# Optimization experiments

Measured on AMD Instinct MI355X. Metric: run time of the kernel, lower is better.

## Reference

```python
import jax, jax.numpy as jnp
import numpy as np
from jax.scipy.special import logsumexp

TAU = 0.07
LAMBDA_LL = 1.0
LAMBDA_GL = 0.5
LAMBDA_SMOOTH = 0.1
NEG_INF = -jnp.inf


def setup_inputs() -> dict:
    key = jax.random.key(0)
    k1, k2, k3, k4 = jax.random.split(key, 4)
    B, L, D, K = 16, 32, 256, 131072
    return {
        "z_t": jax.random.normal(k1, (B, L, D), dtype=jnp.float32),
        "g": jax.random.normal(k2, (B, D), dtype=jnp.float32),
        "va_values": jax.random.uniform(k3, (B, L, 2), dtype=jnp.float32),
        "memory_queue": jax.random.normal(k4, (K, D), dtype=jnp.float32),
    }


def _combined_loss(z_t, g, memory_queue):
    B, L, D = z_t.shape
    N = B * L
    z = z_t.reshape(N, D)

    # ---- Global-Local loss: anchor g[b], positive z_t[b,t], negatives = frames of other clips + queue
    sim_gz = (g @ z.T) / TAU                      # [B, N]
    pos_gl = sim_gz.reshape(B, B, L)[jnp.arange(B), jnp.arange(B)]  # [B, L]
    col_batch = jnp.arange(N) // L                # batch id of each frame column
    neg_gl = jnp.where(col_batch[None, :] == jnp.arange(B)[:, None], NEG_INF, sim_gz)  # [B, N]
    q_gl = (g @ memory_queue.T) / TAU             # [B, K]
    lse_neg_gl = jnp.logaddexp(logsumexp(neg_gl, axis=1), logsumexp(q_gl, axis=1))     # [B]
    loss_gl = jnp.mean(jnp.logaddexp(pos_gl, lse_neg_gl[:, None]) - pos_gl)

    # ---- Local-Local loss: anchor (b,t), positive (b,t+1), negatives = all other frames + queue
    anchor_idx = (jnp.arange(B)[:, None] * L + jnp.arange(L - 1)[None, :]).reshape(-1)  # [M]
    M = anchor_idx.shape[0]
    sim_zz = (z @ z.T) / TAU                      # [N, N]
    rows = sim_zz[anchor_idx]                     # [M, N]
    pos_ll = sim_zz[anchor_idx, anchor_idx + 1]   # [M]
    r = jnp.arange(M)
    neg_rows = rows.at[r, anchor_idx].set(NEG_INF).at[r, anchor_idx + 1].set(NEG_INF)
    q_ll = (z[anchor_idx] @ memory_queue.T) / TAU  # [M, K] -- dominant memory traffic
    lse_neg_ll = jnp.logaddexp(logsumexp(neg_rows, axis=1), logsumexp(q_ll, axis=1))
    loss_ll = jnp.mean(jnp.logaddexp(pos_ll, lse_neg_ll) - pos_ll)
    # NOTE: the VA-derived positive weight in the original code is applied after
    # the logits are built, so it has no effect on the loss; reproduced faithfully.

    # ---- Smoothness loss
    diff = z_t[:, 1:, :] - z_t[:, :-1, :]
    loss_smooth = jnp.mean(jnp.sum(diff * diff, axis=-1))

    total = LAMBDA_LL * loss_ll + LAMBDA_GL * loss_gl + LAMBDA_SMOOTH * loss_smooth
    return total


def reference(z_t, g, va_values, memory_queue):
    # va_values is unused by the effective math (see note in _combined_loss)
    return _combined_loss(z_t, g, memory_queue)
```

## Files before the change

kernel.cpp:

```cpp
#include <hip/hip_runtime.h>
#include <hip/hip_bf16.h>

#define D_ 256
#define NROWS_Z 512
#define NROWS 528
#define KQ 131072
#define NBLK 256
#define NBLK_BIG 512
#define KC 512
#define SUBT 32
#define SCALE_A (14.285714285714286f * 1.4426950408889634f)
#define LN2 0.6931471805599453f

typedef __attribute__((ext_vector_type(8))) short short8;
typedef __attribute__((ext_vector_type(4))) float f32x4;

__device__ __forceinline__ float exp2fast(float x) {
  float r; asm("v_exp_f32 %0, %1" : "=v"(r) : "v"(x)); return r;
}
__device__ __forceinline__ float log2fast(float x) {
  float r; asm("v_log_f32 %0, %1" : "=v"(r) : "v"(x)); return r;
}

__device__ __forceinline__ short bf16r(float x) {
  union { float f; unsigned u; } c; c.f = x;
  unsigned r = (c.u + 0x7fffu + ((c.u >> 16) & 1u)) >> 16;
  return (short)r;
}

__device__ __forceinline__ void merge_ms(float& m, float& s, float m2, float s2) {
  float mm = fmaxf(m, m2);
  s = s * exp2fast(m - mm) + s2 * exp2fast(m2 - mm);
  m = mm;
}

__device__ __forceinline__ void upd(float& m, float& s, float v) {
  float d = v - m;
  if (__builtin_expect(__any(d > 8.f), 0)) {
    const float mn = fmaxf(m, v);
    s *= exp2fast(m - mn);
    m = mn; d = v - m;
  }
  s += exp2fast(d);
}

__device__ __forceinline__ short8 cvt8(float4 a, float4 b) {
  union { unsigned u[4]; short8 s; } o;
  asm("v_cvt_pk_bf16_f32 %0, %1, %2" : "=v"(o.u[0]) : "v"(a.x), "v"(a.y));
  asm("v_cvt_pk_bf16_f32 %0, %1, %2" : "=v"(o.u[1]) : "v"(a.z), "v"(a.w));
  asm("v_cvt_pk_bf16_f32 %0, %1, %2" : "=v"(o.u[2]) : "v"(b.x), "v"(b.y));
  asm("v_cvt_pk_bf16_f32 %0, %1, %2" : "=v"(o.u[3]) : "v"(b.z), "v"(b.w));
  return o.s;
}

__global__ void prep_kernel(const float* __restrict__ z, const float* __restrict__ g,
                            short* __restrict__ Abf, short* __restrict__ Zp,
                            float* __restrict__ smoothp) {
  const int r = blockIdx.x, d = threadIdx.x;
  const float v = (r < NROWS_Z) ? z[r * D_ + d] : g[(r - NROWS_Z) * D_ + d];
  Abf[r * D_ + d] = bf16r(v * SCALE_A);
  if (r < NROWS_Z) {
    Zp[r * D_ + d] = bf16r(v);
    float acc = 0.f;
    if ((r & 31) != 31) { const float dv = z[(r + 1) * D_ + d] - v; acc = dv * dv; }
#pragma unroll
    for (int mask = 1; mask < 64; mask <<= 1) acc += __shfl_xor(acc, mask);
    __shared__ float red[4];
    if ((d & 63) == 0) red[d >> 6] = acc;
    __syncthreads();
    if (d == 0) smoothp[r] = red[0] + red[1] + red[2] + red[3];
  }
}

__global__ __launch_bounds__(512, 2) void big_kernel(
    const float* __restrict__ queue, const short* __restrict__ Abf,
    float2* __restrict__ zpart, float2* __restrict__ gpart) {
  const int tid = threadIdx.x;
  const int chunk = blockIdx.x & 255;
  const int rowgroup = blockIdx.x >> 8;
  const int wid = tid >> 6, lane = tid & 63;
  const int l15 = lane & 15, l4 = lane >> 4;

  __shared__ __align__(16) char qs[2][16 * 512];
  __shared__ float2 gbuf[8 * 16];

  short8 afrag[2][8];
#pragma unroll
  for (int s = 0; s < 2; ++s) {
    const short* base = Abf + (rowgroup * 256 + wid * 32 + s * 16 + l15) * D_ + l4 * 8;
#pragma unroll
    for (int k = 0; k < 8; ++k) afrag[s][k] = *(const short8*)(base + k * 32);
  }
  const short* gbase = Abf + (NROWS_Z + l15) * D_ + l4 * 8;

  float mz[2][4], sz[2][4];
#pragma unroll
  for (int s = 0; s < 2; ++s)
#pragma unroll
    for (int r = 0; r < 4; ++r) { mz[s][r] = -1e30f; sz[s][r] = 0.f; }
  float mg[4], sg[4];
#pragma unroll
  for (int r = 0; r < 4; ++r) { mg[r] = -1e30f; sg[r] = 0.f; }

  const int srow = tid >> 5;
  const int sslot = tid & 31;
  const int woff = srow * 512 + (((sslot ^ srow) & 31) << 4);
  const float* qbase = queue + (size_t)(chunk * KC + srow) * D_ + sslot * 8;

  const f32x4 fz = {0.f, 0.f, 0.f, 0.f};
  const bool dog = (rowgroup == 0);

  float4 fa0 = *(const float4*)qbase;
  float4 fa1 = *(const float4*)(qbase + 4);
  float4 fb0 = *(const float4*)(qbase + 16 * D_);
  float4 fb1 = *(const float4*)(qbase + 16 * D_ + 4);
  *(short8*)(qs[0] + woff) = cvt8(fa0, fa1);
  __syncthreads();

#define COMPUTE(BUF, ST)                                                              \
  {                                                                                   \
    const char* qb = qs[BUF];                                                         \
    f32x4 acc0 = fz, acc1 = fz;                                                       \
    if (dog && ((ST) & 7) == wid) {                                                   \
      f32x4 accg = fz;                                                                \
      _Pragma("unroll")                                                               \
      for (int k = 0; k < 8; ++k) {                                                   \
        const short8 bf = *(const short8*)(qb + l15 * 512 + ((((k * 4 + l4) ^ l15) & 31) << 4)); \
        acc0 = __builtin_amdgcn_mfma_f32_16x16x32_bf16(afrag[0][k], bf, acc0, 0, 0, 0); \
        acc1 = __builtin_amdgcn_mfma_f32_16x16x32_bf16(afrag[1][k], bf, acc1, 0, 0, 0); \
        const short8 ag = *(const short8*)(gbase + k * 32);                           \
        accg = __builtin_amdgcn_mfma_f32_16x16x32_bf16(ag, bf, accg, 0, 0, 0);        \
      }                                                                               \
      _Pragma("unroll")                                                               \
      for (int r = 0; r < 4; ++r) upd(mg[r], sg[r], accg[r]);                         \
    } else {                                                                          \
      _Pragma("unroll")                                                               \
      for (int k = 0; k < 8; ++k) {                                                   \
        const short8 bf = *(const short8*)(qb + l15 * 512 + ((((k * 4 + l4) ^ l15) & 31) << 4)); \
        acc0 = __builtin_amdgcn_mfma_f32_16x16x32_bf16(afrag[0][k], bf, acc0, 0, 0, 0); \
        acc1 = __builtin_amdgcn_mfma_f32_16x16x32_bf16(afrag[1][k], bf, acc1, 0, 0, 0); \
      }                                                                               \
    }                                                                                 \
    _Pragma("unroll")                                                                 \
    for (int r = 0; r < 4; ++r) upd(mz[0][r], sz[0][r], acc0[r]);                     \
    _Pragma("unroll")                                                                 \
    for (int r = 0; r < 4; ++r) upd(mz[1][r], sz[1][r], acc1[r]);                     \
  }

  for (int st = 0; st < SUBT; st += 2) {
    if (st + 2 < SUBT) {
      const float* qp = qbase + (st + 2) * (16 * D_);
      fa0 = *(const float4*)qp;
      fa1 = *(const float4*)(qp + 4);
    }
    *(short8*)(qs[1] + woff) = cvt8(fb0, fb1);
    COMPUTE(0, st)
    __syncthreads();

    if (st + 3 < SUBT) {
      const float* qp = qbase + (st + 3) * (16 * D_);
      fb0 = *(const float4*)qp;
      fb1 = *(const float4*)(qp + 4);
    }
    if (st + 2 < SUBT) *(short8*)(qs[0] + woff) = cvt8(fa0, fa1);
    COMPUTE(1, st + 1)
    __syncthreads();
  }

#pragma unroll
  for (int s = 0; s < 2; ++s)
#pragma unroll
    for (int r = 0; r < 4; ++r) {
#pragma unroll
      for (int mask = 1; mask < 16; mask <<= 1) {
        const float om = __shfl_xor(mz[s][r], mask);
        const float os = __shfl_xor(sz[s][r], mask);
        merge_ms(mz[s][r], sz[s][r], om, os);
      }
    }

  if (l15 == 0) {
#pragma unroll
    for (int s = 0; s < 2; ++s)
#pragma unroll
      for (int r = 0; r < 4; ++r) {
        const int row = rowgroup * 256 + wid * 32 + s * 16 + l4 * 4 + r;
        zpart[row * NBLK + chunk] = make_float2(mz[s][r], sz[s][r]);
      }
  }

  if (dog) {
#pragma unroll
    for (int r = 0; r < 4; ++r) {
#pragma unroll
      for (int mask = 1; mask < 16; mask <<= 1) {
        const float om = __shfl_xor(mg[r], mask);
        const float os = __shfl_xor(sg[r], mask);
        merge_ms(mg[r], sg[r], om, os);
      }
    }
    if (l15 == 0) {
#pragma unroll
      for (int r = 0; r < 4; ++r)
        gbuf[wid * 16 + l4 * 4 + r] = make_float2(mg[r], sg[r]);
    }
    __syncthreads();
    if (tid < 16) {
      float m = gbuf[tid].x, s = gbuf[tid].y;
      for (int w = 1; w < 8; ++w) merge_ms(m, s, gbuf[w * 16 + tid].x, gbuf[w * 16 + tid].y);
      gpart[tid * NBLK + chunk] = make_float2(m, s);
    }
  }
}

__global__ __launch_bounds__(512) void zmm_kernel(
    const short* __restrict__ Abf, const short* __restrict__ Zp,
    float2* __restrict__ zcol, float* __restrict__ posll, float* __restrict__ posgl) {
  const int tid = threadIdx.x;
  const int wid = tid >> 6, lane = tid & 63;
  const int l15 = lane & 15, l4 = lane >> 4;
  const int r0 = blockIdx.x * 16;

  short8 af[8];
#pragma unroll
  for (int k = 0; k < 8; ++k)
    af[k] = *(const short8*)(Abf + (r0 + l15) * D_ + l4 * 8 + k * 32);

  float m[4], s[4];
#pragma unroll
  for (int r = 0; r < 4; ++r) { m[r] = -1e30f; s[r] = 0.f; }

  for (int st = 0; st < 4; ++st) {
    const int c0 = wid * 64 + st * 16;
    const f32x4 fz = {0.f, 0.f, 0.f, 0.f};
    f32x4 acc = fz;
#pragma unroll
    for (int k = 0; k < 8; ++k) {
      const short8 bq = *(const short8*)(Zp + (c0 + l15) * D_ + l4 * 8 + k * 32);
      acc = __builtin_amdgcn_mfma_f32_16x16x32_bf16(af[k], bq, acc, 0, 0, 0);
    }
#pragma unroll
    for (int r = 0; r < 4; ++r) {
      const int row = r0 + l4 * 4 + r;
      const int col = c0 + l15;
      const float v = acc[r];
      bool masked;
      if (r0 < NROWS_Z) {
        if (col == row + 1) posll[row] = v * LN2;
        masked = (col == row) || (col == row + 1);
      } else {
        const int b = row - NROWS_Z;
        const bool own = ((col >> 5) == b);
        if (own) posgl[col] = v * LN2;
        masked = own;
      }
      if (!masked) upd(m[r], s[r], v);
    }
  }
#pragma unroll
  for (int r = 0; r < 4; ++r) {
#pragma unroll
    for (int mask = 1; mask < 16; mask <<= 1) {
      const float om = __shfl_xor(m[r], mask);
      const float os = __shfl_xor(s[r], mask);
      merge_ms(m[r], s[r], om, os);
    }
  }
  __shared__ float2 lds[8][16];
  if (l15 == 0) {
#pragma unroll
    for (int r = 0; r < 4; ++r) lds[wid][l4 * 4 + r] = make_float2(m[r], s[r]);
  }
  __syncthreads();
  if (tid < 16) {
    float mm = lds[0][tid].x, ss = lds[0][tid].y;
    for (int w = 1; w < 8; ++w) merge_ms(mm, ss, lds[w][tid].x, lds[w][tid].y);
    zcol[r0 + tid] = make_float2(mm, ss);
  }
}

__global__ void reduce_kernel(const float2* __restrict__ zpart, const float2* __restrict__ gpart,
                              const float2* __restrict__ zcol, float* __restrict__ lse_row) {
  const int r = blockIdx.x, tid = threadIdx.x;
  const float2 p = (r < NROWS_Z) ? zpart[r * NBLK + tid] : gpart[(r - NROWS_Z) * NBLK + tid];
  float m = p.x, s = p.y;
  __shared__ float2 red[4];
#pragma unroll
  for (int mask = 1; mask < 64; mask <<= 1) {
    const float om = __shfl_xor(m, mask);
    const float os = __shfl_xor(s, mask);
    merge_ms(m, s, om, os);
  }
  if ((tid & 63) == 0) red[tid >> 6] = make_float2(m, s);
  __syncthreads();
  if (tid == 0) {
    for (int w = 1; w < 4; ++w) merge_ms(m, s, red[w].x, red[w].y);
    const float2 zc = zcol[r];
    merge_ms(m, s, zc.x, zc.y);
    lse_row[r] = LN2 * (m + log2fast(s));
  }
}

__global__ void final_kernel(const float* __restrict__ lse_row, const float* __restrict__ posll,
                             const float* __restrict__ posgl, const float* __restrict__ smoothp,
                             float* __restrict__ out) {
  const int tid = threadIdx.x;
  float a_ll = 0.f, a_gl = 0.f, a_sm = 0.f;
  for (int i = tid; i < 496; i += 256) {
    const int b = i / 31, t = i - b * 31;
    const int a = b * 32 + t;
    const float pos = posll[a], lse = lse_row[a];
    const float d = lse - pos;
    a_ll += (d > 0.f) ? d + log1pf(__expf(-d)) : log1pf(__expf(d));
  }
  for (int i = tid; i < 512; i += 256) {
    const float pos = posgl[i], lse = lse_row[NROWS_Z + (i >> 5)];
    const float d = lse - pos;
    a_gl += (d > 0.f) ? d + log1pf(__expf(-d)) : log1pf(__expf(d));
  }
  for (int i = tid; i < 512; i += 256) a_sm += smoothp[i];

  __shared__ float red[4];
  float sums[3] = {a_ll, a_gl, a_sm};
  float tot[3];
  for (int j = 0; j < 3; ++j) {
    float v = sums[j];
#pragma unroll
    for (int mask = 1; mask < 64; mask <<= 1) v += __shfl_xor(v, mask);
    __syncthreads();
    if ((tid & 63) == 0) red[tid >> 6] = v;
    __syncthreads();
    tot[j] = red[0] + red[1] + red[2] + red[3];
  }
  if (tid == 0)
    out[0] = tot[0] / 496.f + 0.5f * (tot[1] / 512.f) + 0.1f * (tot[2] / 496.f);
}

extern "C" void kernel_launch(void* const* d_in, const int* in_sizes, int n_in,
                              void* d_out, int out_size, void* d_ws, size_t ws_size,
                              hipStream_t stream) {
  const float* z = (const float*)d_in[0];
  const float* g = (const float*)d_in[1];
  const float* queue = (const float*)d_in[3];
  float* out = (float*)d_out;
  char* ws = (char*)d_ws;

  constexpr size_t OFF_A = 0;
  constexpr size_t OFF_ZP = OFF_A + 270336;
  constexpr size_t OFF_ZPART = OFF_ZP + 262144;
  constexpr size_t OFF_GPART = OFF_ZPART + 1048576;
  constexpr size_t OFF_ZCOL = OFF_GPART + 32768;
  constexpr size_t OFF_POSLL = OFF_ZCOL + 4224;
  constexpr size_t OFF_POSGL = OFF_POSLL + 2048;
  constexpr size_t OFF_SM = OFF_POSGL + 2048;
  constexpr size_t OFF_LSE = OFF_SM + 2048;

  short* Abf = (short*)(ws + OFF_A);
  short* Zp = (short*)(ws + OFF_ZP);
  float2* zpart = (float2*)(ws + OFF_ZPART);
  float2* gpart = (float2*)(ws + OFF_GPART);
  float2* zcol = (float2*)(ws + OFF_ZCOL);
  float* posll = (float*)(ws + OFF_POSLL);
  float* posgl = (float*)(ws + OFF_POSGL);
  float* smoothp = (float*)(ws + OFF_SM);
  float* lse_row = (float*)(ws + OFF_LSE);

  prep_kernel<<<NROWS, 256, 0, stream>>>(z, g, Abf, Zp, smoothp);
  big_kernel<<<NBLK_BIG, 512, 0, stream>>>(queue, Abf, zpart, gpart);
  zmm_kernel<<<33, 512, 0, stream>>>(Abf, Zp, zcol, posll, posgl);
  reduce_kernel<<<NROWS, 256, 0, stream>>>(zpart, gpart, zcol, lse_row);
  final_kernel<<<1, 256, 0, stream>>>(lse_row, posll, posgl, smoothp, out);
}
```

Baseline: 122.6 us.

## Switch queue GEMM to FP8 MFMA with all rows per block

The queue-logit GEMM now converts the queue and the scaled activations to FP8 and uses the fp8 MFMA instruction. Each block now covers all 512 z rows, where before two row groups each re-read the same queue chunk, so the queue is read from global memory only once. The g rows are computed alongside in every block. The zmm path reuses the scaled bf16 buffer and rescales its output, and the chunk count adapts to the workspace size. FP8 rounding of logits scaled by 1/tau risks accuracy loss in the logsumexp.

```diff
diff --git a/kernel.cpp b/kernel.cpp
--- a/kernel.cpp
+++ b/kernel.cpp
@@ -5,11 +5,8 @@
 #define NROWS_Z 512
 #define NROWS 528
 #define KQ 131072
-#define NBLK 256
-#define NBLK_BIG 512
-#define KC 512
-#define SUBT 32
-#define SCALE_A (14.285714285714286f * 1.4426950408889634f)
+#define SCALE_A 20.6099291041f
+#define INV_SCALE_A (1.0f / SCALE_A)
 #define LN2 0.6931471805599453f
 
 typedef __attribute__((ext_vector_type(8))) short short8;
@@ -26,6 +23,12 @@
   union { float f; unsigned u; } c; c.f = x;
   unsigned r = (c.u + 0x7fffu + ((c.u >> 16) & 1u)) >> 16;
   return (short)r;
+}
+
+__device__ __forceinline__ unsigned cvt2fp8(float a, float b) {
+  unsigned r;
+  asm("v_cvt_pk_fp8_f32 %0, %1, %2" : "=v"(r) : "v"(a), "v"(b));
+  return r & 0xFFFFu;
 }
 
 __device__ __forceinline__ void merge_ms(float& m, float& s, float m2, float s2) {
@@ -44,131 +47,131 @@
   s += exp2fast(d);
 }
 
-__device__ __forceinline__ short8 cvt8(float4 a, float4 b) {
-  union { unsigned u[4]; short8 s; } o;
-  asm("v_cvt_pk_bf16_f32 %0, %1, %2" : "=v"(o.u[0]) : "v"(a.x), "v"(a.y));
-  asm("v_cvt_pk_bf16_f32 %0, %1, %2" : "=v"(o.u[1]) : "v"(a.z), "v"(a.w));
-  asm("v_cvt_pk_bf16_f32 %0, %1, %2" : "=v"(o.u[2]) : "v"(b.x), "v"(b.y));
-  asm("v_cvt_pk_bf16_f32 %0, %1, %2" : "=v"(o.u[3]) : "v"(b.z), "v"(b.w));
-  return o.s;
-}
-
 __global__ void prep_kernel(const float* __restrict__ z, const float* __restrict__ g,
-                            short* __restrict__ Abf, short* __restrict__ Zp,
+                            short* __restrict__ Abf, char* __restrict__ Abf8,
                             float* __restrict__ smoothp) {
   const int r = blockIdx.x, d = threadIdx.x;
+  __shared__ float vals[256];
+  __shared__ float red[4];
   const float v = (r < NROWS_Z) ? z[r * D_ + d] : g[(r - NROWS_Z) * D_ + d];
-  Abf[r * D_ + d] = bf16r(v * SCALE_A);
-  if (r < NROWS_Z) {
-    Zp[r * D_ + d] = bf16r(v);
-    float acc = 0.f;
-    if ((r & 31) != 31) { const float dv = z[(r + 1) * D_ + d] - v; acc = dv * dv; }
-#pragma unroll
-    for (int mask = 1; mask < 64; mask <<= 1) acc += __shfl_xor(acc, mask);
-    __shared__ float red[4];
-    if ((d & 63) == 0) red[d >> 6] = acc;
-    __syncthreads();
-    if (d == 0) smoothp[r] = red[0] + red[1] + red[2] + red[3];
-  }
+  const float vs = v * SCALE_A;
+  Abf[r * D_ + d] = bf16r(vs);
+  vals[d] = vs;
+  float acc = 0.f;
+  if (r < NROWS_Z && (r & 31) != 31) { const float dv = z[(r + 1) * D_ + d] - v; acc = dv * dv; }
+#pragma unroll
+  for (int mask = 1; mask < 64; mask <<= 1) acc += __shfl_xor(acc, mask);
+  if ((d & 63) == 0) red[d >> 6] = acc;
+  __syncthreads();
+  if (d < 64) {
+    const float4 q = *(const float4*)(vals + d * 4);
+    const unsigned w = cvt2fp8(q.x, q.y) | (cvt2fp8(q.z, q.w) << 16);
+    *(unsigned*)(Abf8 + r * D_ + d * 4) = w;
+  }
+  if (d == 0 && r < NROWS_Z) smoothp[r] = red[0] + red[1] + red[2] + red[3];
 }
 
 __global__ __launch_bounds__(512, 2) void big_kernel(
-    const float* __restrict__ queue, const short* __restrict__ Abf,
-    float2* __restrict__ zpart, float2* __restrict__ gpart) {
-  const int tid = threadIdx.x;
-  const int chunk = blockIdx.x & 255;
-  const int rowgroup = blockIdx.x >> 8;
+    const float* __restrict__ queue, const char* __restrict__ Abf8,
+    float2* __restrict__ zpart, float2* __restrict__ gpart,
+    int nchunk, int subt) {
+  const int tid = threadIdx.x, blk = blockIdx.x;
   const int wid = tid >> 6, lane = tid & 63;
   const int l15 = lane & 15, l4 = lane >> 4;
-
-  __shared__ __align__(16) char qs[2][16 * 512];
-  __shared__ float2 gbuf[8 * 16];
-
-  short8 afrag[2][8];
-#pragma unroll
-  for (int s = 0; s < 2; ++s) {
-    const short* base = Abf + (rowgroup * 256 + wid * 32 + s * 16 + l15) * D_ + l4 * 8;
-#pragma unroll
-    for (int k = 0; k < 8; ++k) afrag[s][k] = *(const short8*)(base + k * 32);
-  }
-  const short* gbase = Abf + (NROWS_Z + l15) * D_ + l4 * 8;
-
-  float mz[2][4], sz[2][4];
-#pragma unroll
-  for (int s = 0; s < 2; ++s)
+  const int qrows = KQ / nchunk;
+
+  __shared__ __align__(16) char qs[2][16 * 256];
+  __shared__ float2 gbuf[8][16];
+
+  long afrag[4][8];
+#pragma unroll
+  for (int s = 0; s < 4; ++s) {
+    const char* base = Abf8 + (wid * 64 + s * 16 + l15) * D_ + l4 * 8;
+#pragma unroll
+    for (int k = 0; k < 8; ++k) afrag[s][k] = *(const long*)(base + k * 32);
+  }
+  const char* gBbase = Abf8 + (NROWS_Z + l15) * D_ + l4 * 8;
+
+  float mz[4][4], sz[4][4];
+#pragma unroll
+  for (int s = 0; s < 4; ++s)
 #pragma unroll
     for (int r = 0; r < 4; ++r) { mz[s][r] = -1e30f; sz[s][r] = 0.f; }
-  float mg[4], sg[4];
-#pragma unroll
-  for (int r = 0; r < 4; ++r) { mg[r] = -1e30f; sg[r] = 0.f; }
+  float mg = -1e30f, sg = 0.f;
 
   const int srow = tid >> 5;
   const int sslot = tid & 31;
-  const int woff = srow * 512 + (((sslot ^ srow) & 31) << 4);
-  const float* qbase = queue + (size_t)(chunk * KC + srow) * D_ + sslot * 8;
+  const int woff = srow * D_ + ((sslot ^ srow) << 3);
+  const float* qbase = queue + (size_t)(blk * qrows + srow) * D_ + sslot * 8;
 
   const f32x4 fz = {0.f, 0.f, 0.f, 0.f};
-  const bool dog = (rowgroup == 0);
-
-  float4 fa0 = *(const float4*)qbase;
-  float4 fa1 = *(const float4*)(qbase + 4);
-  float4 fb0 = *(const float4*)(qbase + 16 * D_);
-  float4 fb1 = *(const float4*)(qbase + 16 * D_ + 4);
-  *(short8*)(qs[0] + woff) = cvt8(fa0, fa1);
-  __syncthreads();
+
+#define STAGE(BUF)                                                                    \
+  {                                                                                   \
+    const unsigned w0 = cvt2fp8(fa0.x, fa0.y) | (cvt2fp8(fa0.z, fa0.w) << 16);        \
+    const unsigned w1 = cvt2fp8(fa1.x, fa1.y) | (cvt2fp8(fa1.z, fa1.w) << 16);        \
+    *(uint2*)(qs[BUF] + woff) = make_uint2(w0, w1);                                   \
+  }
 
 #define COMPUTE(BUF, ST)                                                              \
   {                                                                                   \
     const char* qb = qs[BUF];                                                         \
-    f32x4 acc0 = fz, acc1 = fz;                                                       \
-    if (dog && ((ST) & 7) == wid) {                                                   \
+    f32x4 acc0 = fz, acc1 = fz, acc2 = fz, acc3 = fz;                                 \
+    _Pragma("unroll")                                                                 \
+    for (int kk = 0; kk < 8; ++kk) {                                                  \
+      const long bf = *(const long*)(qb + l15 * D_ + (((kk * 4 + l4) ^ l15) << 3));   \
+      acc0 = __builtin_amdgcn_mfma_f32_16x16x32_fp8_fp8(afrag[0][kk], bf, acc0, 0, 0, 0); \
+      acc1 = __builtin_amdgcn_mfma_f32_16x16x32_fp8_fp8(afrag[1][kk], bf, acc1, 0, 0, 0); \
+      acc2 = __builtin_amdgcn_mfma_f32_16x16x32_fp8_fp8(afrag[2][kk], bf, acc2, 0, 0, 0); \
+      acc3 = __builtin_amdgcn_mfma_f32_16x16x32_fp8_fp8(afrag[3][kk], bf, acc3, 0, 0, 0); \
+    }                                                                                 \
+    _Pragma("unroll")                                                                 \
+    for (int r = 0; r < 4; ++r) {                                                     \
+      upd(mz[0][r], sz[0][r], acc0[r]);                                               \
+      upd(mz[1][r], sz[1][r], acc1[r]);                                               \
+      upd(mz[2][r], sz[2][r], acc2[r]);                                               \
+      upd(mz[3][r], sz[3][r], acc3[r]);                                               \
+    }                                                                                 \
+    if ((((ST) & 7)) == wid) {                                                        \
       f32x4 accg = fz;                                                                \
       _Pragma("unroll")                                                               \
-      for (int k = 0; k < 8; ++k) {                                                   \
-        const short8 bf = *(const short8*)(qb + l15 * 512 + ((((k * 4 + l4) ^ l15) & 31) << 4)); \
-        acc0 = __builtin_amdgcn_mfma_f32_16x16x32_bf16(afrag[0][k], bf, acc0, 0, 0, 0); \
-        acc1 = __builtin_amdgcn_mfma_f32_16x16x32_bf16(afrag[1][k], bf, acc1, 0, 0, 0); \
-        const short8 ag = *(const short8*)(gbase + k * 32);                           \
-        accg = __builtin_amdgcn_mfma_f32_16x16x32_bf16(ag, bf, accg, 0, 0, 0);        \
+      for (int kk = 0; kk < 8; ++kk) {                                                \
+        const long bf = *(const long*)(qb + l15 * D_ + (((kk * 4 + l4) ^ l15) << 3)); \
+        const long gb = *(const long*)(gBbase + kk * 32);                             \
+        accg = __builtin_amdgcn_mfma_f32_16x16x32_fp8_fp8(bf, gb, accg, 0, 0, 0);     \
       }                                                                               \
       _Pragma("unroll")                                                               \
-      for (int r = 0; r < 4; ++r) upd(mg[r], sg[r], accg[r]);                         \
-    } else {                                                                          \
-      _Pragma("unroll")                                                               \
-      for (int k = 0; k < 8; ++k) {                                                   \
-        const short8 bf = *(const short8*)(qb + l15 * 512 + ((((k * 4 + l4) ^ l15) & 31) << 4)); \
-        acc0 = __builtin_amdgcn_mfma_f32_16x16x32_bf16(afrag[0][k], bf, acc0, 0, 0, 0); \
-        acc1 = __builtin_amdgcn_mfma_f32_16x16x32_bf16(afrag[1][k], bf, acc1, 0, 0, 0); \
-      }                                                                               \
+      for (int r = 0; r < 4; ++r) upd(mg, sg, accg[r]);                               \
     }                                                                                 \
-    _Pragma("unroll")                                                                 \
-    for (int r = 0; r < 4; ++r) upd(mz[0][r], sz[0][r], acc0[r]);                     \
-    _Pragma("unroll")                                                                 \
-    for (int r = 0; r < 4; ++r) upd(mz[1][r], sz[1][r], acc1[r]);                     \
-  }
-
-  for (int st = 0; st < SUBT; st += 2) {
-    if (st + 2 < SUBT) {
-      const float* qp = qbase + (st + 2) * (16 * D_);
+  }
+
+  float4 fa0 = *(const float4*)qbase;
+  float4 fa1 = *(const float4*)(qbase + 4);
+  STAGE(0)
+  __syncthreads();
+
+  for (int st = 0; st < subt; st += 2) {
+    {
+      const float* qp = qbase + (size_t)(st + 1) * (16 * D_);
       fa0 = *(const float4*)qp;
       fa1 = *(const float4*)(qp + 4);
     }
-    *(short8*)(qs[1] + woff) = cvt8(fb0, fb1);
     COMPUTE(0, st)
+    STAGE(1)
     __syncthreads();
 
-    if (st + 3 < SUBT) {
-      const float* qp = qbase + (st + 3) * (16 * D_);
-      fb0 = *(const float4*)qp;
-      fb1 = *(const float4*)(qp + 4);
-    }
-    if (st + 2 < SUBT) *(short8*)(qs[0] + woff) = cvt8(fa0, fa1);
+    if (st + 2 < subt) {
+      const float* qp = qbase + (size_t)(st + 2) * (16 * D_);
+      fa0 = *(const float4*)qp;
+      fa1 = *(const float4*)(qp + 4);
+    }
     COMPUTE(1, st + 1)
+    if (st + 2 < subt) STAGE(0)
     __syncthreads();
   }
 
 #pragma unroll
-  for (int s = 0; s < 2; ++s)
+  for (int s = 0; s < 4; ++s)
 #pragma unroll
     for (int r = 0; r < 4; ++r) {
 #pragma unroll
@@ -178,43 +181,33 @@
         merge_ms(mz[s][r], sz[s][r], om, os);
       }
     }
-
   if (l15 == 0) {
 #pragma unroll
-    for (int s = 0; s < 2; ++s)
+    for (int s = 0; s < 4; ++s)
 #pragma unroll
       for (int r = 0; r < 4; ++r) {
-        const int row = rowgroup * 256 + wid * 32 + s * 16 + l4 * 4 + r;
-        zpart[row * NBLK + chunk] = make_float2(mz[s][r], sz[s][r]);
+        const int row = wid * 64 + s * 16 + l4 * 4 + r;
+        zpart[row * nchunk + blk] = make_float2(mz[s][r], sz[s][r]);
       }
   }
 
-  if (dog) {
-#pragma unroll
-    for (int r = 0; r < 4; ++r) {
-#pragma unroll
-      for (int mask = 1; mask < 16; mask <<= 1) {
-        const float om = __shfl_xor(mg[r], mask);
-        const float os = __shfl_xor(sg[r], mask);
-        merge_ms(mg[r], sg[r], om, os);
-      }
-    }
-    if (l15 == 0) {
-#pragma unroll
-      for (int r = 0; r < 4; ++r)
-        gbuf[wid * 16 + l4 * 4 + r] = make_float2(mg[r], sg[r]);
-    }
-    __syncthreads();
-    if (tid < 16) {
-      float m = gbuf[tid].x, s = gbuf[tid].y;
-      for (int w = 1; w < 8; ++w) merge_ms(m, s, gbuf[w * 16 + tid].x, gbuf[w * 16 + tid].y);
-      gpart[tid * NBLK + chunk] = make_float2(m, s);
-    }
+#pragma unroll
+  for (int mask = 16; mask < 64; mask <<= 1) {
+    const float om = __shfl_xor(mg, mask);
+    const float os = __shfl_xor(sg, mask);
+    merge_ms(mg, sg, om, os);
+  }
+  if (lane < 16) gbuf[wid][l15] = make_float2(mg, sg);
+  __syncthreads();
+  if (tid < 16) {
+    float m = gbuf[0][tid].x, s = gbuf[0][tid].y;
+    for (int w = 1; w < 8; ++w) merge_ms(m, s, gbuf[w][tid].x, gbuf[w][tid].y);
+    gpart[tid * nchunk + blk] = make_float2(m, s);
   }
 }
 
 __global__ __launch_bounds__(512) void zmm_kernel(
-    const short* __restrict__ Abf, const short* __restrict__ Zp,
+    const short* __restrict__ Abf,
     float2* __restrict__ zcol, float* __restrict__ posll, float* __restrict__ posgl) {
   const int tid = threadIdx.x;
   const int wid = tid >> 6, lane = tid & 63;
@@ -236,14 +229,14 @@
     f32x4 acc = fz;
 #pragma unroll
     for (int k = 0; k < 8; ++k) {
-      const short8 bq = *(const short8*)(Zp + (c0 + l15) * D_ + l4 * 8 + k * 32);
+      const short8 bq = *(const short8*)(Abf + (c0 + l15) * D_ + l4 * 8 + k * 32);
       acc = __builtin_amdgcn_mfma_f32_16x16x32_bf16(af[k], bq, acc, 0, 0, 0);
     }
 #pragma unroll
     for (int r = 0; r < 4; ++r) {
       const int row = r0 + l4 * 4 + r;
       const int col = c0 + l15;
-      const float v = acc[r];
+      const float v = acc[r] * INV_SCALE_A;
       bool masked;
       if (r0 < NROWS_Z) {
         if (col == row + 1) posll[row] = v * LN2;
@@ -280,11 +273,12 @@
 }
 
 __global__ void reduce_kernel(const float2* __restrict__ zpart, const float2* __restrict__ gpart,
-                              const float2* __restrict__ zcol, float* __restrict__ lse_row) {
+                              const float2* __restrict__ zcol, float* __restrict__ lse_row,
+                              int nchunk) {
   const int r = blockIdx.x, tid = threadIdx.x;
-  const float2 p = (r < NROWS_Z) ? zpart[r * NBLK + tid] : gpart[(r - NROWS_Z) * NBLK + tid];
+  const float2 p = (r < NROWS_Z) ? zpart[r * nchunk + tid] : gpart[(r - NROWS_Z) * nchunk + tid];
   float m = p.x, s = p.y;
-  __shared__ float2 red[4];
+  __shared__ float2 red[8];
 #pragma unroll
   for (int mask = 1; mask < 64; mask <<= 1) {
     const float om = __shfl_xor(m, mask);
@@ -294,7 +288,8 @@
   if ((tid & 63) == 0) red[tid >> 6] = make_float2(m, s);
   __syncthreads();
   if (tid == 0) {
-    for (int w = 1; w < 4; ++w) merge_ms(m, s, red[w].x, red[w].y);
+    const int nw = blockDim.x >> 6;
+    for (int w = 1; w < nw; ++w) merge_ms(m, s, red[w].x, red[w].y);
     const float2 zc = zcol[r];
     merge_ms(m, s, zc.x, zc.y);
     lse_row[r] = LN2 * (m + log2fast(s));
@@ -345,29 +340,35 @@
   float* out = (float*)d_out;
   char* ws = (char*)d_ws;
 
-  constexpr size_t OFF_A = 0;
-  constexpr size_t OFF_ZP = OFF_A + 270336;
-  constexpr size_t OFF_ZPART = OFF_ZP + 262144;
-  constexpr size_t OFF_GPART = OFF_ZPART + 1048576;
-  constexpr size_t OFF_ZCOL = OFF_GPART + 32768;
-  constexpr size_t OFF_POSLL = OFF_ZCOL + 4224;
-  constexpr size_t OFF_POSGL = OFF_POSLL + 2048;
-  constexpr size_t OFF_SM = OFF_POSGL + 2048;
-  constexpr size_t OFF_LSE = OFF_SM + 2048;
-
-  short* Abf = (short*)(ws + OFF_A);
-  short* Zp = (short*)(ws + OFF_ZP);
-  float2* zpart = (float2*)(ws + OFF_ZPART);
-  float2* gpart = (float2*)(ws + OFF_GPART);
-  float2* zcol = (float2*)(ws + OFF_ZCOL);
-  float* posll = (float*)(ws + OFF_POSLL);
-  float* posgl = (float*)(ws + OFF_POSGL);
-  float* smoothp = (float*)(ws + OFF_SM);
-  float* lse_row = (float*)(ws + OFF_LSE);
-
-  prep_kernel<<<NROWS, 256, 0, stream>>>(z, g, Abf, Zp, smoothp);
-  big_kernel<<<NBLK_BIG, 512, 0, stream>>>(queue, Abf, zpart, gpart);
-  zmm_kernel<<<33, 512, 0, stream>>>(Abf, Zp, zcol, posll, posgl);
-  reduce_kernel<<<NROWS, 256, 0, stream>>>(zpart, gpart, zcol, lse_row);
+  const size_t offA = 0;
+  const size_t offA8 = 270336;
+  const size_t offZpart = offA8 + 135168;
+  auto need = [&](int nc) -> size_t {
+    return offZpart + (size_t)512 * nc * 8 + (size_t)16 * nc * 8 + 4224 + 2048 + 2048 + 2048 + 2112;
+  };
+  const int nchunk = (ws_size >= need(512)) ? 512 : 256;
+  const int subt = (KQ / nchunk) / 16;
+
+  const size_t offGpart = offZpart + (size_t)512 * nchunk * 8;
+  const size_t offZcol = offGpart + (size_t)16 * nchunk * 8;
+  const size_t offPosll = offZcol + 4224;
+  const size_t offPosgl = offPosll + 2048;
+  const size_t offSm = offPosgl + 2048;
+  const size_t offLse = offSm + 2048;
+
+  short* Abf = (short*)(ws + offA);
+  char* Abf8 = (char*)(ws + offA8);
+  float2* zpart = (float2*)(ws + offZpart);
+  float2* gpart = (float2*)(ws + offGpart);
+  float2* zcol = (float2*)(ws + offZcol);
+  float* posll = (float*)(ws + offPosll);
+  float* posgl = (float*)(ws + offPosgl);
+  float* smoothp = (float*)(ws + offSm);
+  float* lse_row = (float*)(ws + offLse);
+
+  prep_kernel<<<NROWS, 256, 0, stream>>>(z, g, Abf, Abf8, smoothp);
+  big_kernel<<<nchunk, 512, 0, stream>>>(queue, Abf8, zpart, gpart, nchunk, subt);
+  zmm_kernel<<<33, 512, 0, stream>>>(Abf, zcol, posll, posgl);
+  reduce_kernel<<<NROWS, nchunk, 0, stream>>>(zpart, gpart, zcol, lse_row, nchunk);
   final_kernel<<<1, 256, 0, stream>>>(lse_row, posll, posgl, smoothp, out);
 }
```

Result: faster. 118.3 us (-3.6%).
